# Optimization experiments

Measured on AMD Instinct MI355X. Metric: run time of the kernel, lower is better.

## Reference

```python
import jax, jax.numpy as jnp
import numpy as np
from jax import lax

D_MODEL, D_INNER, N_STATE, DT_RANK, K = 1024, 2048, 16, 64, 3
B_SZ, SEQ = 2, 1024

def silu(v):
    return v * jax.nn.sigmoid(v)

def setup_inputs() -> dict:
    key = jax.random.key(0)
    ks = jax.random.split(key, 12)
    s = 0.02
    return {
        'x': jax.random.normal(ks[0], (B_SZ, SEQ, D_MODEL), jnp.float32),
        'A_log': jax.random.normal(ks[1], (D_INNER, N_STATE), jnp.float32) * 0.5,
        'W_in': jax.random.normal(ks[2], (D_MODEL, 2 * D_INNER), jnp.float32) * s,
        'b_in': jax.random.normal(ks[3], (2 * D_INNER,), jnp.float32) * s,
        'conv_w': jax.random.normal(ks[4], (D_INNER, 1, K), jnp.float32) * s,  # depthwise [O,I/g,K]
        'conv_b': jax.random.normal(ks[5], (D_INNER,), jnp.float32) * s,
        'W_x': jax.random.normal(ks[6], (D_INNER, DT_RANK + 2 * N_STATE), jnp.float32) * s,
        'W_dt': jax.random.normal(ks[7], (DT_RANK, D_INNER), jnp.float32) * s,
        'b_dt': jax.random.normal(ks[8], (D_INNER,), jnp.float32) * s,
        'W_out': jax.random.normal(ks[9], (D_INNER, D_MODEL), jnp.float32) * s,
        'b_out': jax.random.normal(ks[10], (D_MODEL,), jnp.float32) * s,
    }

def selective_scan(u, delta, A, B, C):
    # u, delta: [b,l,d]; A: [d,n]; B, C: [b,l,n]
    deltaA = jnp.exp(jnp.einsum('bld,dn->bldn', delta, A))          # [b,l,d,n]
    deltaBu = jnp.einsum('bld,bln,bld->bldn', delta, B, u)           # [b,l,d,n]
    h0 = jnp.zeros((u.shape[0], u.shape[2], A.shape[1]), u.dtype)    # [b,d,n]
    def step(h, inp):
        dA_t, dBu_t, C_t = inp
        h = dA_t * h + dBu_t
        y = jnp.einsum('bdn,bn->bd', h, C_t)
        return h, y
    xs = (jnp.moveaxis(deltaA, 1, 0), jnp.moveaxis(deltaBu, 1, 0), jnp.moveaxis(C, 1, 0))
    _, ys = lax.scan(step, h0, xs)                                   # [l,b,d]
    return jnp.moveaxis(ys, 0, 1)                                    # [b,l,d]

def reference(x, A_log, W_in, b_in, conv_w, conv_b, W_x, W_dt, b_dt, W_out, b_out):
    xr = x @ W_in + b_in                                             # [b,l,2*d_inner]
    u, res = jnp.split(xr, 2, axis=-1)
    # causal depthwise conv1d (pad left k-1, truncate == torch pad=k-1 then slice)
    uc = lax.conv_general_dilated(
        jnp.moveaxis(u, 1, 2), conv_w, window_strides=(1,),
        padding=[(K - 1, 0)], feature_group_count=D_INNER,
        dimension_numbers=('NCH', 'OIH', 'NCH'))
    u = silu(jnp.moveaxis(uc, 2, 1) + conv_b)                        # [b,l,d_inner]
    xp = u @ W_x                                                     # [b,l,dt_rank+2n]
    dt, Bm, Cm = jnp.split(xp, [DT_RANK, DT_RANK + N_STATE], axis=-1)
    delta = jax.nn.softplus(dt @ W_dt + b_dt)                        # [b,l,d_inner]
    A = -jnp.exp(A_log)                                              # [d_inner,n]
    y = selective_scan(u, delta, A, Bm, Cm)                          # [b,l,d_inner]
    y = y * silu(res)
    return y @ W_out + b_out
```

## Files before the change

kernel.cpp:

```cpp
#include <hip/hip_runtime.h>

#define D_MODEL 1024
#define D_INNER 2048
#define N_ST    16
#define DT_RANK 64
#define BSZ     2
#define SEQL    1024
#define NTOK    (BSZ*SEQL)
#define NC      64
#define LC      (SEQL/NC)

typedef __attribute__((ext_vector_type(4))) float f32x4;
typedef __attribute__((ext_vector_type(8))) short bf16x8;

__device__ __forceinline__ short f2b(float f) {
  unsigned u = __builtin_bit_cast(unsigned, f);
  u += 0x7fffu + ((u >> 16) & 1u);
  return (short)(u >> 16);
}

__device__ __forceinline__ float b2f(unsigned short s) {
  return __builtin_bit_cast(float, (unsigned)s << 16);
}

__device__ __forceinline__ void gload16(const void* g, void* l) {
  __builtin_amdgcn_global_load_lds(
      (const __attribute__((address_space(1))) void*)g,
      (__attribute__((address_space(3))) void*)l, 16, 0, 0);
}

template<int SOFTPLUS, int PARTIAL, int RESSPLIT>
__global__ __launch_bounds__(256)
void gemm_kernel(const short* __restrict__ A, const short* __restrict__ Bm,
                 const float* __restrict__ bias, float* __restrict__ C,
                 short* __restrict__ resb,
                 int M, int N, int K, int lda, int ldb, int ldc, int kChunk)
{
  __shared__ short sA[128 * 64];
  __shared__ short sB[128 * 64];
  const int tid  = threadIdx.x;
  const int lane = tid & 63;
  const int wave = tid >> 6;
  const int wr = wave >> 1, wc = wave & 1;
  const int lr = lane & 15, lg = lane >> 4;
  const int m0 = blockIdx.y * 128;
  const int n0 = blockIdx.x * 128;
  const int kStart = blockIdx.z * kChunk;
  int kEnd = kStart + kChunk; if (kEnd > K) kEnd = K;

  if (PARTIAL) C += (size_t)blockIdx.z * M * ldc;

  const int srow = lane >> 3;
  const int scol = ((lane & 7) ^ srow) * 8;
  const short* aS = A + (size_t)(m0 + wave * 32 + srow) * lda + scol + kStart;
  const short* bS = Bm + (size_t)(n0 + wave * 32 + srow) * ldb + scol + kStart;
  short* aD = &sA[wave * 32 * 64];
  short* bD = &sB[wave * 32 * 64];

  f32x4 acc[4][4];
#pragma unroll
  for (int i = 0; i < 4; ++i)
#pragma unroll
    for (int j = 0; j < 4; ++j) acc[i][j] = (f32x4){0.f, 0.f, 0.f, 0.f};

  for (int k0 = kStart; k0 < kEnd; k0 += 64) {
    __syncthreads();
#pragma unroll
    for (int i = 0; i < 4; ++i) {
      gload16(aS + (size_t)(i * 8) * lda, aD + i * 512);
      gload16(bS + (size_t)(i * 8) * ldb, bD + i * 512);
    }
    aS += 64; bS += 64;
    __syncthreads();

#pragma unroll
    for (int kk = 0; kk < 2; ++kk) {
      bf16x8 aF[4], bF[4];
#pragma unroll
      for (int mi = 0; mi < 4; ++mi) {
        const int row = wr * 64 + mi * 16 + lr;
        aF[mi] = *reinterpret_cast<const bf16x8*>(
            &sA[row * 64 + (((kk * 4 + lg) ^ (lr & 7)) * 8)]);
      }
#pragma unroll
      for (int ni = 0; ni < 4; ++ni) {
        const int row = wc * 64 + ni * 16 + lr;
        bF[ni] = *reinterpret_cast<const bf16x8*>(
            &sB[row * 64 + (((kk * 4 + lg) ^ (lr & 7)) * 8)]);
      }
#pragma unroll
      for (int mi = 0; mi < 4; ++mi)
#pragma unroll
        for (int ni = 0; ni < 4; ++ni)
          acc[mi][ni] = __builtin_amdgcn_mfma_f32_16x16x32_bf16(
              aF[mi], bF[ni], acc[mi][ni], 0, 0, 0);
    }
  }

#pragma unroll
  for (int mi = 0; mi < 4; ++mi) {
    const int row = m0 + wr * 64 + mi * 16 + lg * 4;
#pragma unroll
    for (int ni = 0; ni < 4; ++ni) {
      const int col = n0 + wc * 64 + ni * 16 + lr;
      if (RESSPLIT && col >= 2048) {
        const float bv = bias[col];
#pragma unroll
        for (int j = 0; j < 4; ++j) {
          float v = acc[mi][ni][j] + bv;
          resb[(size_t)(row + j) * 2048 + (col - 2048)] =
              f2b(v / (1.f + __expf(-v)));
        }
      } else if (col < N) {
        float bv = (bias != nullptr && blockIdx.z == 0) ? bias[col] : 0.f;
#pragma unroll
        for (int j = 0; j < 4; ++j) {
          float v = acc[mi][ni][j] + bv;
          if (SOFTPLUS) v = fmaxf(v, 0.f) + log1pf(__expf(-fabsf(v)));
          C[(size_t)(row + j) * ldc + col] = v;
        }
      }
    }
  }
}

__device__ __forceinline__ void trans_body(const float* __restrict__ in,
                                           short* __restrict__ out,
                                           int R, int C, int bx, int by,
                                           short (*t)[33], int tidx)
{
  const int c0 = bx * 32, r0 = by * 32;
  const int cc = tidx & 31, rr = tidx >> 5;
#pragma unroll
  for (int i = 0; i < 4; ++i)
    t[rr + i * 8][cc] = f2b(in[(size_t)(r0 + rr + i * 8) * C + c0 + cc]);
  __syncthreads();
#pragma unroll
  for (int i = 0; i < 4; ++i)
    out[(size_t)(c0 + rr + i * 8) * R + r0 + cc] = t[cc][rr + i * 8];
}

#define PB_CAST  2048
#define PB_WIN   4096
#define PB_WX    192
#define PB_WDT   128
#define PB_WOUT  2048

__global__ __launch_bounds__(256)
void prep_kernel(const float* __restrict__ x,    const float* __restrict__ W_in,
                 const float* __restrict__ W_x,  const float* __restrict__ W_dt,
                 const float* __restrict__ W_out,
                 short* __restrict__ xb,  short* __restrict__ Wib,
                 short* __restrict__ Wxb, short* __restrict__ Wdtb,
                 short* __restrict__ Wob)
{
  __shared__ short t[32][33];
  const int bid = blockIdx.x, tidx = threadIdx.x;
  if (bid < PB_CAST) {
    const int i = bid * 256 + tidx;
    float4 v = *reinterpret_cast<const float4*>(x + (size_t)i * 4);
    *reinterpret_cast<short4*>(xb + (size_t)i * 4) =
        make_short4(f2b(v.x), f2b(v.y), f2b(v.z), f2b(v.w));
  } else if (bid < PB_CAST + PB_WIN) {
    const int b = bid - PB_CAST;
    trans_body(W_in, Wib, 1024, 4096, b % 128, b / 128, t, tidx);
  } else if (bid < PB_CAST + PB_WIN + PB_WX) {
    const int b = bid - PB_CAST - PB_WIN;
    trans_body(W_x, Wxb, 2048, 96, b % 3, b / 3, t, tidx);
  } else if (bid < PB_CAST + PB_WIN + PB_WX + PB_WDT) {
    const int b = bid - PB_CAST - PB_WIN - PB_WX;
    trans_body(W_dt, Wdtb, 64, 2048, b % 64, b / 64, t, tidx);
  } else {
    const int b = bid - PB_CAST - PB_WIN - PB_WX - PB_WDT;
    trans_body(W_out, Wob, 2048, 1024, b % 32, b / 32, t, tidx);
  }
}

__global__ __launch_bounds__(256)
void combine8_kernel(const float* __restrict__ part, float* __restrict__ xp,
                     short* __restrict__ dtb)
{
  const int gid = blockIdx.x * 256 + threadIdx.x;
  const int r = gid / 24, q = gid - r * 24;
  float4 s = make_float4(0.f, 0.f, 0.f, 0.f);
#pragma unroll
  for (int c = 0; c < 8; ++c) {
    const float4 v = *reinterpret_cast<const float4*>(
        part + (size_t)c * 2048 * 96 + (size_t)r * 96 + q * 4);
    s.x += v.x; s.y += v.y; s.z += v.z; s.w += v.w;
  }
  *reinterpret_cast<float4*>(xp + (size_t)r * 96 + q * 4) = s;
  if (q < 16)
    *reinterpret_cast<short4*>(dtb + (size_t)r * 64 + q * 4) =
        make_short4(f2b(s.x), f2b(s.y), f2b(s.z), f2b(s.w));
}

__global__ __launch_bounds__(256)
void combine4_kernel(const float* __restrict__ part, const float* __restrict__ bias,
                     float* __restrict__ out)
{
  const int gid = blockIdx.x * 256 + threadIdx.x;
  const int r = gid >> 8, c4 = gid & 255;
  const float4 bv = *reinterpret_cast<const float4*>(bias + c4 * 4);
  float4 s = bv;
#pragma unroll
  for (int z = 0; z < 4; ++z) {
    const float4 v = *reinterpret_cast<const float4*>(
        part + (size_t)z * 2048 * 1024 + (size_t)r * 1024 + c4 * 4);
    s.x += v.x; s.y += v.y; s.z += v.z; s.w += v.w;
  }
  *reinterpret_cast<float4*>(out + (size_t)r * 1024 + c4 * 4) = s;
}

__global__ __launch_bounds__(256)
void conv_silu_kernel(const float* __restrict__ up, const float* __restrict__ cw,
                      const float* __restrict__ cb, short* __restrict__ ub)
{
  int i  = blockIdx.x * 256 + threadIdx.x;
  int t  = i >> 9;
  int dq = (i & 511) << 2;
  int l  = t & (SEQL - 1);
  float4 w0 = *reinterpret_cast<const float4*>(cw + dq * 3);
  float4 w1 = *reinterpret_cast<const float4*>(cw + dq * 3 + 4);
  float4 w2 = *reinterpret_cast<const float4*>(cw + dq * 3 + 8);
  float4 bb = *reinterpret_cast<const float4*>(cb + dq);
  float4 x2 = *reinterpret_cast<const float4*>(up + (size_t)t * 2048 + dq);
  float4 x1 = (l >= 1) ? *reinterpret_cast<const float4*>(up + (size_t)(t - 1) * 2048 + dq)
                       : make_float4(0.f, 0.f, 0.f, 0.f);
  float4 x0 = (l >= 2) ? *reinterpret_cast<const float4*>(up + (size_t)(t - 2) * 2048 + dq)
                       : make_float4(0.f, 0.f, 0.f, 0.f);
  float r0 = bb.x + w0.x * x0.x + w0.y * x1.x + w0.z * x2.x;
  float r1 = bb.y + w0.w * x0.y + w1.x * x1.y + w1.y * x2.y;
  float r2 = bb.z + w1.z * x0.z + w1.w * x1.z + w2.x * x2.z;
  float r3 = bb.w + w2.y * x0.w + w2.z * x1.w + w2.w * x2.w;
  float o0 = r0 / (1.f + __expf(-r0));
  float o1 = r1 / (1.f + __expf(-r1));
  float o2 = r2 / (1.f + __expf(-r2));
  float o3 = r3 / (1.f + __expf(-r3));
  *reinterpret_cast<short4*>(ub + (size_t)t * 2048 + dq) =
      make_short4(f2b(o0), f2b(o1), f2b(o2), f2b(o3));
}

__global__ __launch_bounds__(256, 4)
void scan_pass1(const float* __restrict__ delta, const unsigned short* __restrict__ ub,
                const float* __restrict__ xp, const float* __restrict__ A_log,
                float* __restrict__ sdl, float* __restrict__ HS)
{
  const int d = blockIdx.y * 256 + threadIdx.x;
  const int c = blockIdx.x, b = blockIdx.z;
  const int t0 = (b << 10) + c * LC;
  float Ac[16];
#pragma unroll
  for (int q = 0; q < 4; ++q) {
    float4 a = *reinterpret_cast<const float4*>(A_log + (size_t)d * 16 + q * 4);
    Ac[q * 4 + 0] = -__expf(a.x); Ac[q * 4 + 1] = -__expf(a.y);
    Ac[q * 4 + 2] = -__expf(a.z); Ac[q * 4 + 3] = -__expf(a.w);
  }
  float h[16];
#pragma unroll
  for (int n = 0; n < 16; ++n) h[n] = 0.f;
  float sd = 0.f;
  const float* dp = delta + (size_t)t0 * 2048 + d;
  const unsigned short* up = ub + (size_t)t0 * 2048 + d;
  const float* xb = xp + (size_t)t0 * 96 + DT_RANK;
#pragma unroll 4
  for (int t = 0; t < LC; ++t) {
    float dl = dp[(size_t)t * 2048];
    float ul = b2f(up[(size_t)t * 2048]);
    float Bf[16];
#pragma unroll
    for (int q = 0; q < 4; ++q)
      *reinterpret_cast<float4*>(&Bf[q * 4]) =
          *reinterpret_cast<const float4*>(xb + (size_t)t * 96 + q * 4);
    float dlu = dl * ul;
    sd += dl;
#pragma unroll
    for (int n = 0; n < 16; ++n)
      h[n] = __expf(dl * Ac[n]) * h[n] + dlu * Bf[n];
  }
  sdl[((size_t)b * NC + c) * 2048 + d] = sd;
  float* hs = HS + (((size_t)b * NC + c) * 2048 + d) * 16;
#pragma unroll
  for (int q = 0; q < 4; ++q)
    *reinterpret_cast<float4*>(hs + q * 4) =
        make_float4(h[q * 4], h[q * 4 + 1], h[q * 4 + 2], h[q * 4 + 3]);
}

__global__ __launch_bounds__(256)
void scan_pass2(const float* __restrict__ sdl, const float* __restrict__ A_log,
                float* __restrict__ HS)
{
  const int gid = blockIdx.x * 256 + threadIdx.x;
  const int b = gid >> 15, rest = gid & 32767;
  const int d = rest >> 4;
  const float Ac = -__expf(A_log[rest]);
  float h = 0.f;
  for (int c = 0; c < NC; ++c) {
    const size_t idx = (((size_t)b * NC + c) << 15) + rest;
    float S = HS[idx];
    float sd = sdl[((size_t)b * NC + c) * 2048 + d];
    HS[idx] = h;
    h = __expf(sd * Ac) * h + S;
  }
}

__global__ __launch_bounds__(256, 4)
void scan_pass3(const float* __restrict__ delta, const unsigned short* __restrict__ ub,
                const float* __restrict__ xp, const float* __restrict__ A_log,
                const float* __restrict__ HS, const unsigned short* __restrict__ rb,
                short* __restrict__ zb)
{
  const int d = blockIdx.y * 256 + threadIdx.x;
  const int c = blockIdx.x, b = blockIdx.z;
  const int t0 = (b << 10) + c * LC;
  float Ac[16];
#pragma unroll
  for (int q = 0; q < 4; ++q) {
    float4 a = *reinterpret_cast<const float4*>(A_log + (size_t)d * 16 + q * 4);
    Ac[q * 4 + 0] = -__expf(a.x); Ac[q * 4 + 1] = -__expf(a.y);
    Ac[q * 4 + 2] = -__expf(a.z); Ac[q * 4 + 3] = -__expf(a.w);
  }
  float h[16];
  const float* hs = HS + (((size_t)b * NC + c) * 2048 + d) * 16;
#pragma unroll
  for (int q = 0; q < 4; ++q) {
    float4 v = *reinterpret_cast<const float4*>(hs + q * 4);
    h[q * 4 + 0] = v.x; h[q * 4 + 1] = v.y; h[q * 4 + 2] = v.z; h[q * 4 + 3] = v.w;
  }
  const float* dp = delta + (size_t)t0 * 2048 + d;
  const unsigned short* up = ub + (size_t)t0 * 2048 + d;
  const float* xb = xp + (size_t)t0 * 96 + DT_RANK;
  const float* xc = xp + (size_t)t0 * 96 + DT_RANK + N_ST;
  const unsigned short* rp = rb + (size_t)t0 * 2048 + d;
  short* zp = zb + (size_t)t0 * 2048 + d;
#pragma unroll 4
  for (int t = 0; t < LC; ++t) {
    float dl = dp[(size_t)t * 2048];
    float ul = b2f(up[(size_t)t * 2048]);
    float rv = b2f(rp[(size_t)t * 2048]);
    float Bf[16], Cf[16];
#pragma unroll
    for (int q = 0; q < 4; ++q) {
      *reinterpret_cast<float4*>(&Bf[q * 4]) =
          *reinterpret_cast<const float4*>(xb + (size_t)t * 96 + q * 4);
      *reinterpret_cast<float4*>(&Cf[q * 4]) =
          *reinterpret_cast<const float4*>(xc + (size_t)t * 96 + q * 4);
    }
    float dlu = dl * ul;
    float p0 = 0.f, p1 = 0.f, p2 = 0.f, p3 = 0.f;
#pragma unroll
    for (int n = 0; n < 16; ++n) {
      h[n] = __expf(dl * Ac[n]) * h[n] + dlu * Bf[n];
      float t2 = h[n] * Cf[n];
      if ((n & 3) == 0) p0 += t2;
      else if ((n & 3) == 1) p1 += t2;
      else if ((n & 3) == 2) p2 += t2;
      else p3 += t2;
    }
    float p = (p0 + p1) + (p2 + p3);
    zp[(size_t)t * 2048] = f2b(p * rv);
  }
}

extern "C" void kernel_launch(void* const* d_in, const int* in_sizes, int n_in,
                              void* d_out, int out_size, void* d_ws, size_t ws_size,
                              hipStream_t stream)
{
  const float* x      = (const float*)d_in[0];
  const float* A_log  = (const float*)d_in[1];
  const float* W_in   = (const float*)d_in[2];
  const float* b_in   = (const float*)d_in[3];
  const float* conv_w = (const float*)d_in[4];
  const float* conv_b = (const float*)d_in[5];
  const float* W_x    = (const float*)d_in[6];
  const float* W_dt   = (const float*)d_in[7];
  const float* b_dt   = (const float*)d_in[8];
  const float* W_out  = (const float*)d_in[9];
  const float* b_out  = (const float*)d_in[10];
  float* out = (float*)d_out;

  char* p = (char*)d_ws;
  float* xr     = (float*)p; p += (size_t)NTOK * 2048 * 4;
  short* rb     = (short*)p; p += (size_t)NTOK * 2048 * 2;
  short* ub     = (short*)p; p += (size_t)NTOK * 2048 * 2;
  float* xp     = (float*)p; p += (size_t)NTOK * 96 * 4;
  short* dtb    = (short*)p; p += (size_t)NTOK * 64 * 2;
  float* delta  = (float*)p; p += (size_t)NTOK * 2048 * 4;
  short* zb     = (short*)p; p += (size_t)NTOK * 2048 * 2;
  short* xb     = (short*)p; p += (size_t)NTOK * 1024 * 2;
  short* Wib    = (short*)p; p += (size_t)4096 * 1024 * 2;
  short* Wxb    = (short*)p; p += (size_t)128 * 2048 * 2;
  short* Wdtb   = (short*)p; p += (size_t)2048 * 64 * 2;
  short* Wob    = (short*)p; p += (size_t)1024 * 2048 * 2;
  float* xppart = (float*)p; p += (size_t)8 * 2048 * 96 * 4;
  float* opart  = (float*)p; p += (size_t)4 * 2048 * 1024 * 4;
  float* sdl    = (float*)p; p += (size_t)BSZ * NC * 2048 * 4;
  float* HS     = (float*)p; p += (size_t)BSZ * NC * 2048 * 16 * 4;

  prep_kernel<<<dim3(PB_CAST + PB_WIN + PB_WX + PB_WDT + PB_WOUT), 256, 0, stream>>>(
      x, W_in, W_x, W_dt, W_out, xb, Wib, Wxb, Wdtb, Wob);

  gemm_kernel<0, 0, 1><<<dim3(32, 16, 1), 256, 0, stream>>>(
      xb, Wib, b_in, xr, rb, NTOK, 4096, 1024, 1024, 1024, 2048, 1024);
  conv_silu_kernel<<<dim3(4096), 256, 0, stream>>>(xr, conv_w, conv_b, ub);
  gemm_kernel<0, 1, 0><<<dim3(1, 16, 8), 256, 0, stream>>>(
      ub, Wxb, nullptr, xppart, nullptr, NTOK, 96, 2048, 2048, 2048, 96, 256);
  combine8_kernel<<<dim3(192), 256, 0, stream>>>(xppart, xp, dtb);
  gemm_kernel<1, 0, 0><<<dim3(16, 16, 1), 256, 0, stream>>>(
      dtb, Wdtb, b_dt, delta, nullptr, NTOK, 2048, 64, 64, 64, 2048, 64);
  scan_pass1<<<dim3(NC, 8, BSZ), 256, 0, stream>>>(
      delta, (const unsigned short*)ub, xp, A_log, sdl, HS);
  scan_pass2<<<dim3(256), 256, 0, stream>>>(sdl, A_log, HS);
  scan_pass3<<<dim3(NC, 8, BSZ), 256, 0, stream>>>(
      delta, (const unsigned short*)ub, xp, A_log, HS, (const unsigned short*)rb, zb);
  gemm_kernel<0, 1, 0><<<dim3(8, 16, 4), 256, 0, stream>>>(
      zb, Wob, nullptr, opart, nullptr, NTOK, 1024, 2048, 2048, 2048, 1024, 512);
  combine4_kernel<<<dim3(2048), 256, 0, stream>>>(opart, b_out, out);
}
```

Baseline: 159.5 us.

## Double-buffer GEMM LDS tiles, store in_proj u half as bf16, deepen W_x split-K

```diff
diff --git a/kernel.cpp b/kernel.cpp
--- a/kernel.cpp
+++ b/kernel.cpp
@@ -33,11 +33,11 @@
 __global__ __launch_bounds__(256)
 void gemm_kernel(const short* __restrict__ A, const short* __restrict__ Bm,
                  const float* __restrict__ bias, float* __restrict__ C,
-                 short* __restrict__ resb,
+                 short* __restrict__ upb, short* __restrict__ resb,
                  int M, int N, int K, int lda, int ldb, int ldc, int kChunk)
 {
-  __shared__ short sA[128 * 64];
-  __shared__ short sB[128 * 64];
+  __shared__ short sA[2][128 * 64];
+  __shared__ short sB[2][128 * 64];
   const int tid  = threadIdx.x;
   const int lane = tid & 63;
   const int wave = tid >> 6;
@@ -47,6 +47,7 @@
   const int n0 = blockIdx.x * 128;
   const int kStart = blockIdx.z * kChunk;
   int kEnd = kStart + kChunk; if (kEnd > K) kEnd = K;
+  const int nt = (kEnd - kStart) >> 6;
 
   if (PARTIAL) C += (size_t)blockIdx.z * M * ldc;
 
@@ -54,8 +55,16 @@
   const int scol = ((lane & 7) ^ srow) * 8;
   const short* aS = A + (size_t)(m0 + wave * 32 + srow) * lda + scol + kStart;
   const short* bS = Bm + (size_t)(n0 + wave * 32 + srow) * ldb + scol + kStart;
-  short* aD = &sA[wave * 32 * 64];
-  short* bD = &sB[wave * 32 * 64];
+  const int ldsOff = wave * 2048;
+
+#define STAGE(buf, koff)                                                   \
+  {                                                                        \
+    _Pragma("unroll")                                                      \
+    for (int i_ = 0; i_ < 4; ++i_) {                                       \
+      gload16(aS + (size_t)(i_ * 8) * lda + (koff), &sA[buf][ldsOff + i_ * 512]); \
+      gload16(bS + (size_t)(i_ * 8) * ldb + (koff), &sB[buf][ldsOff + i_ * 512]); \
+    }                                                                      \
+  }
 
   f32x4 acc[4][4];
 #pragma unroll
@@ -63,15 +72,12 @@
 #pragma unroll
     for (int j = 0; j < 4; ++j) acc[i][j] = (f32x4){0.f, 0.f, 0.f, 0.f};
 
-  for (int k0 = kStart; k0 < kEnd; k0 += 64) {
-    __syncthreads();
-#pragma unroll
-    for (int i = 0; i < 4; ++i) {
-      gload16(aS + (size_t)(i * 8) * lda, aD + i * 512);
-      gload16(bS + (size_t)(i * 8) * ldb, bD + i * 512);
-    }
-    aS += 64; bS += 64;
-    __syncthreads();
+  STAGE(0, 0);
+  __syncthreads();
+
+  for (int t = 0; t < nt; ++t) {
+    const int cur = t & 1;
+    if (t + 1 < nt) STAGE(cur ^ 1, (t + 1) * 64);
 
 #pragma unroll
     for (int kk = 0; kk < 2; ++kk) {
@@ -80,13 +86,13 @@
       for (int mi = 0; mi < 4; ++mi) {
         const int row = wr * 64 + mi * 16 + lr;
         aF[mi] = *reinterpret_cast<const bf16x8*>(
-            &sA[row * 64 + (((kk * 4 + lg) ^ (lr & 7)) * 8)]);
+            &sA[cur][row * 64 + (((kk * 4 + lg) ^ (lr & 7)) * 8)]);
       }
 #pragma unroll
       for (int ni = 0; ni < 4; ++ni) {
         const int row = wc * 64 + ni * 16 + lr;
         bF[ni] = *reinterpret_cast<const bf16x8*>(
-            &sB[row * 64 + (((kk * 4 + lg) ^ (lr & 7)) * 8)]);
+            &sB[cur][row * 64 + (((kk * 4 + lg) ^ (lr & 7)) * 8)]);
       }
 #pragma unroll
       for (int mi = 0; mi < 4; ++mi)
@@ -95,7 +101,9 @@
           acc[mi][ni] = __builtin_amdgcn_mfma_f32_16x16x32_bf16(
               aF[mi], bF[ni], acc[mi][ni], 0, 0, 0);
     }
-  }
+    __syncthreads();
+  }
+#undef STAGE
 
 #pragma unroll
   for (int mi = 0; mi < 4; ++mi) {
@@ -103,13 +111,19 @@
 #pragma unroll
     for (int ni = 0; ni < 4; ++ni) {
       const int col = n0 + wc * 64 + ni * 16 + lr;
-      if (RESSPLIT && col >= 2048) {
+      if (RESSPLIT) {
         const float bv = bias[col];
-#pragma unroll
-        for (int j = 0; j < 4; ++j) {
-          float v = acc[mi][ni][j] + bv;
-          resb[(size_t)(row + j) * 2048 + (col - 2048)] =
-              f2b(v / (1.f + __expf(-v)));
+        if (col < 2048) {
+#pragma unroll
+          for (int j = 0; j < 4; ++j)
+            upb[(size_t)(row + j) * 2048 + col] = f2b(acc[mi][ni][j] + bv);
+        } else {
+#pragma unroll
+          for (int j = 0; j < 4; ++j) {
+            float v = acc[mi][ni][j] + bv;
+            resb[(size_t)(row + j) * 2048 + (col - 2048)] =
+                f2b(v / (1.f + __expf(-v)));
+          }
         }
       } else if (col < N) {
         float bv = (bias != nullptr && blockIdx.z == 0) ? bias[col] : 0.f;
@@ -177,14 +191,14 @@
 }
 
 __global__ __launch_bounds__(256)
-void combine8_kernel(const float* __restrict__ part, float* __restrict__ xp,
-                     short* __restrict__ dtb)
+void combine16_kernel(const float* __restrict__ part, float* __restrict__ xp,
+                      short* __restrict__ dtb)
 {
   const int gid = blockIdx.x * 256 + threadIdx.x;
   const int r = gid / 24, q = gid - r * 24;
   float4 s = make_float4(0.f, 0.f, 0.f, 0.f);
 #pragma unroll
-  for (int c = 0; c < 8; ++c) {
+  for (int c = 0; c < 16; ++c) {
     const float4 v = *reinterpret_cast<const float4*>(
         part + (size_t)c * 2048 * 96 + (size_t)r * 96 + q * 4);
     s.x += v.x; s.y += v.y; s.z += v.z; s.w += v.w;
@@ -213,7 +227,7 @@
 }
 
 __global__ __launch_bounds__(256)
-void conv_silu_kernel(const float* __restrict__ up, const float* __restrict__ cw,
+void conv_silu_kernel(const unsigned short* __restrict__ up, const float* __restrict__ cw,
                       const float* __restrict__ cb, short* __restrict__ ub)
 {
   int i  = blockIdx.x * 256 + threadIdx.x;
@@ -224,15 +238,14 @@
   float4 w1 = *reinterpret_cast<const float4*>(cw + dq * 3 + 4);
   float4 w2 = *reinterpret_cast<const float4*>(cw + dq * 3 + 8);
   float4 bb = *reinterpret_cast<const float4*>(cb + dq);
-  float4 x2 = *reinterpret_cast<const float4*>(up + (size_t)t * 2048 + dq);
-  float4 x1 = (l >= 1) ? *reinterpret_cast<const float4*>(up + (size_t)(t - 1) * 2048 + dq)
-                       : make_float4(0.f, 0.f, 0.f, 0.f);
-  float4 x0 = (l >= 2) ? *reinterpret_cast<const float4*>(up + (size_t)(t - 2) * 2048 + dq)
-                       : make_float4(0.f, 0.f, 0.f, 0.f);
-  float r0 = bb.x + w0.x * x0.x + w0.y * x1.x + w0.z * x2.x;
-  float r1 = bb.y + w0.w * x0.y + w1.x * x1.y + w1.y * x2.y;
-  float r2 = bb.z + w1.z * x0.z + w1.w * x1.z + w2.x * x2.z;
-  float r3 = bb.w + w2.y * x0.w + w2.z * x1.w + w2.w * x2.w;
+  ushort4 X2 = *reinterpret_cast<const ushort4*>(up + (size_t)t * 2048 + dq);
+  ushort4 z4; z4.x = z4.y = z4.z = z4.w = 0;
+  ushort4 X1 = (l >= 1) ? *reinterpret_cast<const ushort4*>(up + (size_t)(t - 1) * 2048 + dq) : z4;
+  ushort4 X0 = (l >= 2) ? *reinterpret_cast<const ushort4*>(up + (size_t)(t - 2) * 2048 + dq) : z4;
+  float r0 = bb.x + w0.x * b2f(X0.x) + w0.y * b2f(X1.x) + w0.z * b2f(X2.x);
+  float r1 = bb.y + w0.w * b2f(X0.y) + w1.x * b2f(X1.y) + w1.y * b2f(X2.y);
+  float r2 = bb.z + w1.z * b2f(X0.z) + w1.w * b2f(X1.z) + w2.x * b2f(X2.z);
+  float r3 = bb.w + w2.y * b2f(X0.w) + w2.z * b2f(X1.w) + w2.w * b2f(X2.w);
   float o0 = r0 / (1.f + __expf(-r0));
   float o1 = r1 / (1.f + __expf(-r1));
   float o2 = r2 / (1.f + __expf(-r2));
@@ -380,7 +393,7 @@
   float* out = (float*)d_out;
 
   char* p = (char*)d_ws;
-  float* xr     = (float*)p; p += (size_t)NTOK * 2048 * 4;
+  short* upb    = (short*)p; p += (size_t)NTOK * 2048 * 2;
   short* rb     = (short*)p; p += (size_t)NTOK * 2048 * 2;
   short* ub     = (short*)p; p += (size_t)NTOK * 2048 * 2;
   float* xp     = (float*)p; p += (size_t)NTOK * 96 * 4;
@@ -392,8 +405,9 @@
   short* Wxb    = (short*)p; p += (size_t)128 * 2048 * 2;
   short* Wdtb   = (short*)p; p += (size_t)2048 * 64 * 2;
   short* Wob    = (short*)p; p += (size_t)1024 * 2048 * 2;
-  float* xppart = (float*)p; p += (size_t)8 * 2048 * 96 * 4;
-  float* opart  = (float*)p; p += (size_t)4 * 2048 * 1024 * 4;
+  float* scr    = (float*)p; p += (size_t)4 * 2048 * 1024 * 4;
+  float* xppart = scr;
+  float* opart  = scr;
   float* sdl    = (float*)p; p += (size_t)BSZ * NC * 2048 * 4;
   float* HS     = (float*)p; p += (size_t)BSZ * NC * 2048 * 16 * 4;
 
@@ -401,19 +415,20 @@
       x, W_in, W_x, W_dt, W_out, xb, Wib, Wxb, Wdtb, Wob);
 
   gemm_kernel<0, 0, 1><<<dim3(32, 16, 1), 256, 0, stream>>>(
-      xb, Wib, b_in, xr, rb, NTOK, 4096, 1024, 1024, 1024, 2048, 1024);
-  conv_silu_kernel<<<dim3(4096), 256, 0, stream>>>(xr, conv_w, conv_b, ub);
-  gemm_kernel<0, 1, 0><<<dim3(1, 16, 8), 256, 0, stream>>>(
-      ub, Wxb, nullptr, xppart, nullptr, NTOK, 96, 2048, 2048, 2048, 96, 256);
-  combine8_kernel<<<dim3(192), 256, 0, stream>>>(xppart, xp, dtb);
+      xb, Wib, b_in, nullptr, upb, rb, NTOK, 4096, 1024, 1024, 1024, 0, 1024);
+  conv_silu_kernel<<<dim3(4096), 256, 0, stream>>>(
+      (const unsigned short*)upb, conv_w, conv_b, ub);
+  gemm_kernel<0, 1, 0><<<dim3(1, 16, 16), 256, 0, stream>>>(
+      ub, Wxb, nullptr, xppart, nullptr, nullptr, NTOK, 96, 2048, 2048, 2048, 96, 128);
+  combine16_kernel<<<dim3(192), 256, 0, stream>>>(xppart, xp, dtb);
   gemm_kernel<1, 0, 0><<<dim3(16, 16, 1), 256, 0, stream>>>(
-      dtb, Wdtb, b_dt, delta, nullptr, NTOK, 2048, 64, 64, 64, 2048, 64);
+      dtb, Wdtb, b_dt, delta, nullptr, nullptr, NTOK, 2048, 64, 64, 64, 2048, 64);
   scan_pass1<<<dim3(NC, 8, BSZ), 256, 0, stream>>>(
       delta, (const unsigned short*)ub, xp, A_log, sdl, HS);
   scan_pass2<<<dim3(256), 256, 0, stream>>>(sdl, A_log, HS);
   scan_pass3<<<dim3(NC, 8, BSZ), 256, 0, stream>>>(
       delta, (const unsigned short*)ub, xp, A_log, HS, (const unsigned short*)rb, zb);
   gemm_kernel<0, 1, 0><<<dim3(8, 16, 4), 256, 0, stream>>>(
-      zb, Wob, nullptr, opart, nullptr, NTOK, 1024, 2048, 2048, 2048, 1024, 512);
+      zb, Wob, nullptr, opart, nullptr, nullptr, NTOK, 1024, 2048, 2048, 2048, 1024, 512);
   combine4_kernel<<<dim3(2048), 256, 0, stream>>>(opart, b_out, out);
 }
```

New measurement: 158.0 us. Within noise of the previous version (-0.9%).
